# Kernel tuning notes

Hardware: AMD Instinct MI355X
Metric: run time of the kernel (lower is better)

## Reference

```python
import jax, jax.numpy as jnp
import numpy as np

LS = 64                      # latent_scaling
TYPES = [8, 1, 1]            # Pyr, SST, VIP widths
DEPTHS = [1, 1, 1]           # L4, L23, L5
B, T = 64, 256
I = 2 * 1 * len(TYPES) * len(DEPTHS)          # 18
AREA = sum(TYPES) * sum(DEPTHS) * LS          # 1920 per area
H = 2 * AREA                                  # 3840


def _build_mask():
    """Block-structured Bernoulli sign mask over 2 areas x (3 layers x 3 types).

    Mirrors the BB* buffers of celltypeRNN: within-area blocks drawn
    Bernoulli(p) with sign +1 for Pyr sources, -1 for SST/VIP sources;
    cross-area blocks zero.
    """
    rng = np.random.default_rng(0)
    # population order per area: (L4,Pyr),(L4,SST),(L4,VIP),(L23,...),(L5,...)
    sizes = [DEPTHS[l] * TYPES[t] * LS for l in range(3) for t in range(3)]
    offs = np.concatenate([[0], np.cumsum(sizes)])
    n_pop = 9
    # connection probability table P[src, dst] (from the source's pvals;
    # unspecified pairs default to 0.05)
    P = np.full((n_pop, n_pop), 0.05)
    # self blocks (diagonal): L4 [.1,.01,.03], L23 [.06,.05,.01], L5 [.04,.03,.03]
    diag = [0.10, 0.01, 0.03, 0.06, 0.05, 0.01, 0.04, 0.03, 0.03]
    for i, p in enumerate(diag):
        P[i, i] = p
    # L4Pyr (idx 0) -> others
    for dst, p in [(1, .04), (4, .04), (7, .03), (2, .00), (5, .02), (8, .11), (3, .07), (6, .00)]:
        P[0, dst] = p
    # L4SST (idx 1) -> others
    for dst, p in [(0, .22), (3, .33), (6, .08), (2, .22), (5, .21), (8, .07), (4, .05), (7, .04)]:
        P[1, dst] = p
    # L4VIP (idx 2) -> Pyr
    P[2, 0] = 0.0
    P[2, 3] = 0.0
    sign = np.array([+1.0, -1.0, -1.0] * 3)  # Pyr +, SST -, VIP -
    mask = np.zeros((H, H), dtype=np.float32)
    for area in range(2):           # V1, LM (within-area connectivity only)
        base = area * AREA
        for s in range(n_pop):
            for d in range(n_pop):
                r0, r1 = base + offs[d], base + offs[d + 1]
                c0, c1 = base + offs[s], base + offs[s + 1]
                blk = (rng.random((r1 - r0, c1 - c0)) < P[s, d]).astype(np.float32)
                mask[r0:r1, c0:c1] = blk * sign[s]
    return jnp.asarray(mask)


def setup_inputs() -> dict:
    key = jax.random.key(0)
    kx, kwi, kbi, kwh, kbh = jax.random.split(key, 5)
    s = 1.0 / np.sqrt(H)
    return {
        "x": jax.random.normal(kx, (B, T, I), jnp.float32),
        "W_ih": jax.random.uniform(kwi, (H, I), jnp.float32, -s, s),
        "b_ih": jax.random.uniform(kbi, (H,), jnp.float32, -s, s),
        "W_hh": jax.random.uniform(kwh, (H, H), jnp.float32, -s, s),
        "b_hh": jax.random.uniform(kbh, (H,), jnp.float32, -s, s),
        "mask": _build_mask(),
    }


def reference(x, W_ih, b_ih, W_hh, b_hh, mask):
    # cell-type connectivity mask applied to the recurrent weights
    Wm = W_hh * mask                              # [H, H]
    # precompute input projection for all timesteps: [B, T, H]
    xp = jnp.einsum("bti,hi->bth", x, W_ih) + b_ih + b_hh
    h0 = jnp.zeros((x.shape[0], Wm.shape[0]), x.dtype)

    def step(h, xp_t):                            # h: [B, H], xp_t: [B, H]
        h = jax.nn.relu(xp_t + h @ Wm.T)
        return h, h

    _, hs = jax.lax.scan(step, h0, jnp.swapaxes(xp, 0, 1))  # [T, B, H]
    return jnp.swapaxes(hs, 0, 1)                            # [B, T, H]
```

## Files before the change

kernel.cpp:

```cpp
#include <hip/hip_runtime.h>
#include <stdint.h>
#include <stddef.h>

#define HH 3840
#define AH 1920
#define NI 18
#define NT 256
#define NBATCH 64
#define KMAX 224
#define JSLOT 28
#define NRW 120
#define NB 8
#define NGROUP 16
#define NBLK_G 16
#define NBLOCKS 256
#define NTHREADS 1024
#define COLS 1920
#define COLT 1938
#define HNEW_PAD 9

#define ENT_BYTES ((size_t)HH * KMAX * 4)
#define CNT_BYTES ((size_t)HH * 4)
#define XT2_BYTES ((size_t)NT * NI * NBATCH * 2)
#define HT_HALF   ((size_t)NGROUP * AH * NB)
#define HT_BYTES  (2 * HT_HALF * 2)
#define FLAG_ELEMS ((size_t)NGROUP * NBLK_G * 32)
#define PC_ELEMS  16

#define SLAB_B    (COLT * 16)
#define OFF_HNEW  (2 * SLAB_B)
#define HNEW_B    (2 * NRW * HNEW_PAD * 4)
#define SMEM_USED (OFF_HNEW + HNEW_B)
#define SMEM_ALLOC 83968

#define AS1 __attribute__((address_space(1)))
#define AS3 __attribute__((address_space(3)))

typedef unsigned long long u64;

__device__ __forceinline__ float lo16(uint32_t u) {
    union { uint16_t q; _Float16 h; } c; c.q = (uint16_t)u; return (float)c.h;
}
__device__ __forceinline__ uint16_t f2h_bits(float f) {
    union { _Float16 h; uint16_t u; } c; c.h = (_Float16)f; return c.u;
}
__device__ __forceinline__ uint32_t pkrtz(float x, float y) {
    typedef __fp16 h2 __attribute__((ext_vector_type(2)));
    union { h2 h; uint32_t u; } c; c.h = __builtin_amdgcn_cvt_pkrtz(x, y); return c.u;
}
__device__ __forceinline__ void gll16(const void* g, void* l) {
    __builtin_amdgcn_global_load_lds((const AS1 uint32_t*)g, (AS3 uint32_t*)l, 16, 0, 0);
}
__device__ __forceinline__ void astore(u64* p, u64 v) {
    __hip_atomic_store(p, v, __ATOMIC_RELAXED, __HIP_MEMORY_SCOPE_AGENT);
}
#define SWZ(v, pat) __uint_as_float(__builtin_amdgcn_ds_swizzle(__float_as_uint(v), pat))
#define DPA(c, ctrl) c += __uint_as_float(__builtin_amdgcn_mov_dpp(__float_as_uint(c), ctrl, 0xF, 0xF, true))
#define FMIX_LO(acc, h2, w) asm("v_fma_mix_f32 %0, %1, %2, %0 op_sel:[0,0,0] op_sel_hi:[1,0,0]" : "+v"(acc) : "v"(h2), "v"(w))
#define FMIX_HI(acc, h2, w) asm("v_fma_mix_f32 %0, %1, %2, %0 op_sel:[1,0,0] op_sel_hi:[1,0,0]" : "+v"(acc) : "v"(h2), "v"(w))

__global__ void init_ws_kernel(uint32_t* __restrict__ flg, uint32_t* __restrict__ ht0) {
    size_t i = (size_t)blockIdx.x * blockDim.x + threadIdx.x;
    if (i < FLAG_ELEMS + PC_ELEMS) flg[i] = 0;
    if (i < HT_HALF / 2) ht0[i] = 0;
}

__global__ void build_ell_kernel(const float* __restrict__ Whh, const float* __restrict__ mask,
                                 const float* __restrict__ Wih,
                                 uint32_t* __restrict__ ent, uint32_t* __restrict__ cnt) {
    int gw = (int)((blockIdx.x * blockDim.x + threadIdx.x) >> 6);
    int lane = threadIdx.x & 63;
    if (gw >= HH) return;
    const int d = gw;
    const int area = (d >= AH) ? 1 : 0;
    const float* mrow = mask + (size_t)d * HH + (size_t)area * AH;
    const float* wrow = Whh + (size_t)d * HH + (size_t)area * AH;
    uint32_t* erow = ent + (size_t)d * KMAX;
    uint32_t base = 0;
    for (int c0 = 0; c0 < AH; c0 += 64) {
        int c = c0 + lane;
        float m = mrow[c];
        bool pred = (m != 0.0f);
        uint64_t mk = __ballot(pred);
        if (pred) {
            uint32_t pos = base + (uint32_t)__popcll(mk & ((1ull << lane) - 1ull));
            if (pos < KMAX) erow[pos] = ((uint32_t)c << 16) | (uint32_t)f2h_bits(wrow[c] * m);
        }
        base += (uint32_t)__popcll(mk);
    }
    if (lane < NI) {
        uint32_t pos = base + (uint32_t)lane;
        if (pos < KMAX)
            erow[pos] = ((uint32_t)(COLS + lane) << 16) | (uint32_t)f2h_bits(Wih[(size_t)d * NI + lane]);
    }
    base += NI;
    if (lane == 0) cnt[d] = (base < KMAX) ? base : KMAX;
}

__global__ void xt_kernel(const float* __restrict__ x, uint16_t* __restrict__ xT2) {
    int i = blockIdx.x * blockDim.x + threadIdx.x;
    if (i >= NT * NI * NBATCH) return;
    int b = i % NBATCH;
    int rest = i / NBATCH;
    int ii = rest % NI;
    int t = rest / NI;
    xT2[i] = f2h_bits(x[((size_t)b * NT + t) * NI + ii]);
}

__global__ __launch_bounds__(NTHREADS, 4) void rnn_kernel(
    const uint32_t* __restrict__ ent, const uint32_t* __restrict__ cnt,
    const uint16_t* __restrict__ xT2, uint16_t* __restrict__ hT,
    uint32_t* __restrict__ flg,
    const float* __restrict__ bih, const float* __restrict__ bhh,
    float* __restrict__ out)
{
    extern __shared__ char smem[];
    uint4* slab = (uint4*)smem;
    float* hnew = (float*)(smem + OFF_HNEW);

    const int tid = threadIdx.x;
    const int G = blockIdx.x & 15, role = blockIdx.x >> 4;
    const int a = G >> 3, g = G & 7;
    const int row0 = role * NRW;
    const size_t mySlot = ((size_t)G * NBLK_G + role) * 32;

    const int wv = tid >> 6, lane = tid & 63;
    const int ro = lane >> 3;
    const int kq = lane & 7;
    const int r  = wv * 8 + ro;

    float wj[JSLOT];
    int   aj[JSLOT];
    float biasr = 0.f;
    int wm = 0;
    if (wv < 15) {
        const int gRow = a * AH + row0 + r;
        const int n = (int)cnt[gRow];
        biasr = bih[gRow] + bhh[gRow];
        int jmax = (n > kq) ? ((n - kq + 7) >> 3) : 0;
        const uint32_t* ep = ent + (size_t)gRow * KMAX;
        #pragma unroll
        for (int j = 0; j < JSLOT; ++j) {
            uint32_t e = (j < jmax) ? ep[kq + 8 * j] : 0u;
            aj[j] = (int)((e >> 16) * 16);
            wj[j] = (j < jmax) ? lo16(e) : 0.0f;
        }
        wm = jmax;
        #pragma unroll
        for (int s = 1; s < 64; s <<= 1) {
            int ov = __shfl_xor(wm, s, 64);
            wm = (ov > wm) ? ov : wm;
        }
    }

    for (int t = 0; t < NT; ++t) {
        const int cur = t & 1, nxt = cur ^ 1;
        if (wv == 0 && lane < NI)
            gll16(xT2 + ((size_t)t * NI + lane) * NBATCH + g * NB,
                  &slab[cur * COLT + COLS + lane]);
        if (wv > 0 || t == 0) {
            const int p = (role + wv) & 15;
            if (t > 0) {
                const uint32_t* sl = flg + ((size_t)G * NBLK_G + p) * 32;
                int guard = 0;
                while (__hip_atomic_load(sl, __ATOMIC_RELAXED, __HIP_MEMORY_SCOPE_AGENT)
                       < (uint32_t)t && ++guard < (1 << 15))
                    __builtin_amdgcn_s_sleep(1);
            }
            const uint4* sp = (const uint4*)(hT + (size_t)cur * HT_HALF
                                             + ((size_t)G * AH + p * NRW) * NB);
            const int l2 = (lane < 56) ? (64 + lane) : lane;
            uint4 v0, v1;
            asm volatile("global_load_dwordx4 %0, %2, off sc0 sc1\n\t"
                         "global_load_dwordx4 %1, %3, off sc0 sc1\n\t"
                         "s_waitcnt vmcnt(0)"
                         : "=&v"(v0), "=&v"(v1)
                         : "v"(sp + lane), "v"(sp + l2)
                         : "memory");
            uint4* dst = slab + cur * COLT + p * NRW;
            dst[lane] = v0;
            dst[l2] = v1;
        }
        __syncthreads();

        if (wv == 15 && t > 0) {
            const float* hp = hnew + ((t - 1) & 1) * NRW * HNEW_PAD;
            for (int i = lane; i < NB * NRW; i += 64) {
                int bb = i / NRW, d = i - bb * NRW;
                out[(((size_t)(g * NB + bb)) * NT + (t - 1)) * HH + (size_t)a * AH + row0 + d]
                    = hp[d * HNEW_PAD + bb];
            }
        }

        if (wv < 15) {
            const char* sb = (const char*)(slab + cur * COLT);
            float c0 = 0.f, c1 = 0.f, c2 = 0.f, c3 = 0.f, c4 = 0.f, c5 = 0.f, c6 = 0.f, c7 = 0.f;
            #pragma unroll
            for (int j = 0; j < JSLOT; ++j) {
                if (j >= wm) break;
                const uint4 hv = *(const uint4*)(sb + aj[j]);
                const float wf = wj[j];
                FMIX_LO(c0, hv.x, wf); FMIX_HI(c1, hv.x, wf);
                FMIX_LO(c2, hv.y, wf); FMIX_HI(c3, hv.y, wf);
                FMIX_LO(c4, hv.z, wf); FMIX_HI(c5, hv.z, wf);
                FMIX_LO(c6, hv.w, wf); FMIX_HI(c7, hv.w, wf);
            }
            c0 += SWZ(c0, 0x101F); c1 += SWZ(c1, 0x101F); c2 += SWZ(c2, 0x101F); c3 += SWZ(c3, 0x101F);
            c4 += SWZ(c4, 0x101F); c5 += SWZ(c5, 0x101F); c6 += SWZ(c6, 0x101F); c7 += SWZ(c7, 0x101F);
            DPA(c0, 0x4E); DPA(c1, 0x4E); DPA(c2, 0x4E); DPA(c3, 0x4E);
            DPA(c4, 0x4E); DPA(c5, 0x4E); DPA(c6, 0x4E); DPA(c7, 0x4E);
            DPA(c0, 0xB1); DPA(c1, 0xB1); DPA(c2, 0xB1); DPA(c3, 0xB1);
            DPA(c4, 0xB1); DPA(c5, 0xB1); DPA(c6, 0xB1); DPA(c7, 0xB1);
            if (kq == 0) {
                float h0 = fmaxf(c0 + biasr, 0.f), h1 = fmaxf(c1 + biasr, 0.f);
                float h2 = fmaxf(c2 + biasr, 0.f), h3 = fmaxf(c3 + biasr, 0.f);
                float h4 = fmaxf(c4 + biasr, 0.f), h5 = fmaxf(c5 + biasr, 0.f);
                float h6 = fmaxf(c6 + biasr, 0.f), h7 = fmaxf(c7 + biasr, 0.f);
                uint4 pk;
                pk.x = pkrtz(h0, h1); pk.y = pkrtz(h2, h3);
                pk.z = pkrtz(h4, h5); pk.w = pkrtz(h6, h7);
                u64* dst8 = (u64*)(hT + (size_t)nxt * HT_HALF
                                   + ((size_t)G * AH + row0 + r) * NB);
                astore(dst8,     ((u64)pk.y << 32) | pk.x);
                astore(dst8 + 1, ((u64)pk.w << 32) | pk.z);
                slab[nxt * COLT + row0 + r] = pk;
                float* hp = hnew + cur * NRW * HNEW_PAD + r * HNEW_PAD;
                hp[0] = h0; hp[1] = h1; hp[2] = h2; hp[3] = h3;
                hp[4] = h4; hp[5] = h5; hp[6] = h6; hp[7] = h7;
            }
        }
        __syncthreads();

        if (tid == 0)
            __hip_atomic_store(flg + mySlot, (uint32_t)(t + 1), __ATOMIC_RELAXED,
                               __HIP_MEMORY_SCOPE_AGENT);
    }
    {
        const float* hp = hnew + ((NT - 1) & 1) * NRW * HNEW_PAD;
        for (int i = tid; i < NB * NRW; i += NTHREADS) {
            int bb = i / NRW, d = i - bb * NRW;
            out[(((size_t)(g * NB + bb)) * NT + (NT - 1)) * HH + (size_t)a * AH + row0 + d]
                = hp[d * HNEW_PAD + bb];
        }
    }
}

extern "C" void kernel_launch(void* const* d_in, const int* in_sizes, int n_in,
                              void* d_out, int out_size, void* d_ws, size_t ws_size,
                              hipStream_t stream)
{
    const float* x    = (const float*)d_in[0];
    const float* Wih  = (const float*)d_in[1];
    const float* bih  = (const float*)d_in[2];
    const float* Whh  = (const float*)d_in[3];
    const float* bhh  = (const float*)d_in[4];
    const float* mask = (const float*)d_in[5];
    float* out = (float*)d_out;

    char* ws = (char*)d_ws;
    uint32_t* ent = (uint32_t*)(ws);
    uint32_t* cnt = (uint32_t*)(ws + ENT_BYTES);
    uint16_t* xT2 = (uint16_t*)(ws + ENT_BYTES + CNT_BYTES);
    uint16_t* hT  = (uint16_t*)(ws + ENT_BYTES + CNT_BYTES + XT2_BYTES);
    uint32_t* flg = (uint32_t*)(ws + ENT_BYTES + CNT_BYTES + XT2_BYTES + HT_BYTES);

    init_ws_kernel<<<512, 256, 0, stream>>>(flg, (uint32_t*)hT);
    build_ell_kernel<<<(HH * 64 + 255) / 256, 256, 0, stream>>>(Whh, mask, Wih, ent, cnt);
    xt_kernel<<<(NT * NI * NBATCH + 255) / 256, 256, 0, stream>>>(x, xT2);

    hipFuncSetAttribute((const void*)rnn_kernel,
                        hipFuncAttributeMaxDynamicSharedMemorySize, SMEM_ALLOC);

    void* args[] = {(void*)&ent, (void*)&cnt, (void*)&xT2, (void*)&hT, (void*)&flg,
                    (void*)&bih, (void*)&bhh, (void*)&out};
    hipLaunchCooperativeKernel((const void*)rnn_kernel, dim3(NBLOCKS), dim3(NTHREADS),
                               args, SMEM_ALLOC, stream);
}
```

Baseline: 1.138 ms.

## Interleave ELL entries across column residue classes to balance bank access

The ELL build now buckets nonzeros by column modulo 8 and interleaves the buckets round-robin in each row's entry list, using per-bucket counts from a first pass. The likely aim is to spread the h-vector column indices read by consecutive entries across different LDS banks or lanes in the recurrent kernel, cutting conflicts in the gather. It adds a second pass over the mask in the one-time build kernel and more complex rank arithmetic.

```diff
diff --git a/kernel.cpp b/kernel.cpp
--- a/kernel.cpp
+++ b/kernel.cpp
@@ -54,6 +54,18 @@
 __device__ __forceinline__ void astore(u64* p, u64 v) {
     __hip_atomic_store(p, v, __ATOMIC_RELAXED, __HIP_MEMORY_SCOPE_AGENT);
 }
+__device__ __forceinline__ uint32_t sel8(const uint32_t v[8], int b) {
+    uint32_t x = v[0];
+    #pragma unroll
+    for (int i = 1; i < 8; ++i) x = (b == i) ? v[i] : x;
+    return x;
+}
+__device__ __forceinline__ u64 sel8_64(const u64 v[8], int b) {
+    u64 x = v[0];
+    #pragma unroll
+    for (int i = 1; i < 8; ++i) x = (b == i) ? v[i] : x;
+    return x;
+}
 #define SWZ(v, pat) __uint_as_float(__builtin_amdgcn_ds_swizzle(__float_as_uint(v), pat))
 #define DPA(c, ctrl) c += __uint_as_float(__builtin_amdgcn_mov_dpp(__float_as_uint(c), ctrl, 0xF, 0xF, true))
 #define FMIX_LO(acc, h2, w) asm("v_fma_mix_f32 %0, %1, %2, %0 op_sel:[0,0,0] op_sel_hi:[1,0,0]" : "+v"(acc) : "v"(h2), "v"(w))
@@ -76,25 +88,52 @@
     const float* mrow = mask + (size_t)d * HH + (size_t)area * AH;
     const float* wrow = Whh + (size_t)d * HH + (size_t)area * AH;
     uint32_t* erow = ent + (size_t)d * KMAX;
-    uint32_t base = 0;
-    for (int c0 = 0; c0 < AH; c0 += 64) {
-        int c = c0 + lane;
-        float m = mrow[c];
-        bool pred = (m != 0.0f);
-        uint64_t mk = __ballot(pred);
+    const u64 below = ((u64)1 << lane) - 1;
+
+    uint32_t sz[8] = {0, 0, 0, 0, 0, 0, 0, 0};
+    for (int c0 = 0; c0 <= AH; c0 += 64) {
+        bool isx = (c0 == AH);
+        bool pred;
+        if (isx) pred = (lane < NI);
+        else     pred = (mrow[c0 + lane] != 0.0f);
+        int b = lane & 7;
+        #pragma unroll
+        for (int bb = 0; bb < 8; ++bb)
+            sz[bb] += (uint32_t)__popcll(__ballot(pred && (b == bb)));
+    }
+    uint32_t run[8] = {0, 0, 0, 0, 0, 0, 0, 0};
+    for (int c0 = 0; c0 <= AH; c0 += 64) {
+        bool isx = (c0 == AH);
+        int col; bool pred; float wval;
+        if (isx) {
+            col = COLS + lane; pred = (lane < NI);
+            wval = pred ? Wih[(size_t)d * NI + lane] : 0.0f;
+        } else {
+            col = c0 + lane;
+            float m = mrow[col];
+            pred = (m != 0.0f);
+            wval = pred ? wrow[col] * m : 0.0f;
+        }
+        int b = lane & 7;
+        u64 bal[8];
+        #pragma unroll
+        for (int bb = 0; bb < 8; ++bb) bal[bb] = __ballot(pred && (b == bb));
         if (pred) {
-            uint32_t pos = base + (uint32_t)__popcll(mk & ((1ull << lane) - 1ull));
-            if (pos < KMAX) erow[pos] = ((uint32_t)c << 16) | (uint32_t)f2h_bits(wrow[c] * m);
-        }
-        base += (uint32_t)__popcll(mk);
-    }
-    if (lane < NI) {
-        uint32_t pos = base + (uint32_t)lane;
-        if (pos < KMAX)
-            erow[pos] = ((uint32_t)(COLS + lane) << 16) | (uint32_t)f2h_bits(Wih[(size_t)d * NI + lane]);
-    }
-    base += NI;
-    if (lane == 0) cnt[d] = (base < KMAX) ? base : KMAX;
+            uint32_t k = sel8(run, b) + (uint32_t)__popcll(sel8_64(bal, b) & below);
+            uint32_t rank = k;
+            #pragma unroll
+            for (int bb = 0; bb < 8; ++bb) {
+                uint32_t cap = (bb < b) ? (k + 1) : k;
+                uint32_t add = (sz[bb] < cap) ? sz[bb] : cap;
+                rank += (bb == b) ? 0u : add;
+            }
+            if (rank < KMAX) erow[rank] = ((uint32_t)col << 16) | (uint32_t)f2h_bits(wval);
+        }
+        #pragma unroll
+        for (int bb = 0; bb < 8; ++bb) run[bb] += (uint32_t)__popcll(bal[bb]);
+    }
+    uint32_t tot = sz[0] + sz[1] + sz[2] + sz[3] + sz[4] + sz[5] + sz[6] + sz[7];
+    if (lane == 0) cnt[d] = (tot < KMAX) ? tot : KMAX;
 }
 
 __global__ void xt_kernel(const float* __restrict__ x, uint16_t* __restrict__ xT2) {
```

Measured after the change: 1.250 ms. 9.8% more time.
